# Kernel tuning notes

Measured on AMD Instinct MI355X. Metric: run time of the kernel, lower is better.

## Reference

```python
import jax, jax.numpy as jnp
import numpy as np

HEADS = 16
DIM_HEAD = 64


def setup_inputs() -> dict:
    key = jax.random.key(0)
    k1, k2, k3, k4 = jax.random.split(key, 4)
    b, sq, skv, dim = 2, 2048, 2048, 1024
    inner = HEADS * DIM_HEAD
    return {
        "x_q": jax.random.normal(k1, (b, sq, dim), dtype=jnp.float32),
        "x_kv": jax.random.normal(k2, (b, skv, dim), dtype=jnp.float32),
        "W_qkv": jax.random.normal(k3, (dim, 3 * inner), dtype=jnp.float32) * (dim ** -0.5),
        "W_out": jax.random.normal(k4, (inner, dim), dtype=jnp.float32) * (inner ** -0.5),
        "b_out": jnp.zeros((dim,), dtype=jnp.float32),
    }


def reference(x_q, x_kv, W_qkv, W_out, b_out):
    b, sq, dim = x_q.shape
    skv = x_kv.shape[1]
    inner = HEADS * DIM_HEAD
    scale = DIM_HEAD ** -0.5
    # to_qkv on concat([x_q, x_kv], seq) as in the original (bias-free linear)
    qkv = jnp.concatenate([x_q, x_kv], axis=1) @ W_qkv  # [b, sq+skv, 3*inner]
    q, k, v = jnp.split(qkv, 3, axis=-1)
    q = q[:, :sq].reshape(b, sq, HEADS, DIM_HEAD).transpose(0, 2, 1, 3)   # [b,h,sq,d]
    k = k[:, sq:].reshape(b, skv, HEADS, DIM_HEAD).transpose(0, 2, 1, 3)  # [b,h,skv,d]
    v = v[:, sq:].reshape(b, skv, HEADS, DIM_HEAD).transpose(0, 2, 1, 3)  # [b,h,skv,d]
    dots = jnp.einsum('bhqd,bhkd->bhqk', q, k) * scale
    attn = jax.nn.softmax(dots, axis=-1)  # dropout p=0.0 -> identity
    out = jnp.einsum('bhqk,bhkd->bhqd', attn, v)
    out = out.transpose(0, 2, 1, 3).reshape(b, sq, inner)
    return out @ W_out + b_out
```

## Files before the change

kernel.cpp:

```cpp
#include <hip/hip_runtime.h>


typedef __attribute__((ext_vector_type(8))) short short8;
typedef __attribute__((ext_vector_type(4))) short short4v;
typedef __attribute__((ext_vector_type(4))) float floatx4;
typedef __attribute__((ext_vector_type(16))) float floatx16;

#define QSCALE 0.18033688f

#if __has_builtin(__builtin_amdgcn_exp2f)
#define EXP2(x) __builtin_amdgcn_exp2f(x)
#else
#define EXP2(x) exp2f(x)
#endif

__device__ __forceinline__ ushort f2b(float f) {
  union { float f; unsigned u; } x; x.f = f;
  unsigned r = (x.u + 0x7fffu + ((x.u >> 16) & 1u)) >> 16;
  return (ushort)r;
}

__device__ __forceinline__ unsigned f2b2(float a, float b) {
  union { float f; unsigned u; } x, y; x.f = a; y.f = b;
  return __builtin_amdgcn_perm(y.u + 0x8000u, x.u + 0x8000u, 0x07060302u);
}

__device__ __forceinline__ unsigned cvtpk(float a, float b) {
  unsigned r;
  asm("v_cvt_pk_bf16_f32 %0, %1, %2" : "=v"(r) : "v"(a), "v"(b));
  return r;
}

#define GLL(gp, lp)                                                            \
  __builtin_amdgcn_global_load_lds(                                            \
      (const __attribute__((address_space(1))) void*)(gp),                     \
      (__attribute__((address_space(3))) void*)(lp), 16, 0, 0)

__global__ void prep(const float* __restrict__ xq, const float* __restrict__ xkv,
                     ushort* __restrict__ oq, ushort* __restrict__ okv,
                     const float* __restrict__ Wqkv, ushort* __restrict__ WqkvT,
                     const float* __restrict__ Wout, ushort* __restrict__ WoutT) {
  __shared__ float tile[32][33];
  int bid = blockIdx.x;
  const int n = 4096 * 1024;
  if (bid < 2048) {
    bool lo = bid < 1024;
    const float* in = lo ? xq : xkv;
    ushort* out = lo ? oq : okv;
    int b2 = lo ? bid : bid - 1024;
    int stride = 1024 * 256 * 4;
    for (int i = (b2 * 256 + (int)threadIdx.x) * 4; i < n; i += stride) {
      float4 v = *(const float4*)(in + i);
      uint2 o;
      o.x = cvtpk(v.x, v.y);
      o.y = cvtpk(v.z, v.w);
      *(uint2*)(out + i) = o;
    }
    return;
  }
  int tb = bid - 2048;
  int bx = tb & 127, by = tb >> 7;
  bool first = bx < 96;
  const float* in = first ? Wqkv : Wout;
  ushort* out = first ? WqkvT : WoutT;
  int N = first ? 3072 : 1024;
  int bxx = first ? bx : bx - 96;
  int k0 = by * 32, n0 = bxx * 32;
  {
    int row = threadIdx.x >> 3, c = threadIdx.x & 7;
    float4 v = *(const float4*)(in + (size_t)(k0 + row) * N + n0 + c * 4);
    tile[row][c * 4 + 0] = v.x;
    tile[row][c * 4 + 1] = v.y;
    tile[row][c * 4 + 2] = v.z;
    tile[row][c * 4 + 3] = v.w;
  }
  __syncthreads();
  {
    int tx2 = threadIdx.x & 15, ty2 = threadIdx.x >> 4;
#pragma unroll
    for (int i = 0; i < 2; i++) {
      int nr = ty2 + 16 * i;
      unsigned v = cvtpk(tile[2 * tx2][nr], tile[2 * tx2 + 1][nr]);
      *(unsigned*)(out + (size_t)(n0 + nr) * 1024 + k0 + 2 * tx2) = v;
    }
  }
}

__global__ __launch_bounds__(256, 3) void gemm_qkv(
    const ushort* __restrict__ Aq, const ushort* __restrict__ Akv,
    const ushort* __restrict__ Bt,
    ushort* __restrict__ Cq, ushort* __restrict__ Ck, ushort* __restrict__ Cv) {
  __shared__ __align__(16) ushort smem[17408];
  ushort* Asb = smem;
  ushort* Bsb = smem + 8192;
  int lid = blockIdx.y * 24 + blockIdx.x;
  int nid = (lid & 7) * 96 + (lid >> 3);
  int bx = nid % 24, by = nid / 24;
  const int n0 = bx * 128, m0 = by * 128;
  const ushort* A = (bx >= 8) ? Akv : Aq;
  const int t = threadIdx.x;
  const int w = t >> 6, lane = t & 63, dl = lane & 15, g = lane >> 4;
  const int wm = (w >> 1) * 64, wn = (w & 1) * 64;
  const int K = 1024;

  auto stage = [&](int buf, int k0) {
#pragma unroll
    for (int p = 0; p < 2; p++) {
      int j = t + p * 256;
      int row = j >> 2, slot = j & 3, c = (slot - row) & 3;
      GLL(A + (size_t)(m0 + row) * K + k0 + c * 8, &Asb[buf * 4096 + j * 8]);
    }
#pragma unroll
    for (int p = 0; p < 2; p++) {
      int j = t + p * 256;
      int row = j >> 2, slot = j & 3, c = (slot - row) & 3;
      GLL(Bt + (size_t)(n0 + row) * K + k0 + c * 8, &Bsb[buf * 4096 + j * 8]);
    }
  };

  const floatx4 fz = {0.f, 0.f, 0.f, 0.f};
  floatx4 acc[4][4];
#pragma unroll
  for (int i = 0; i < 4; i++)
#pragma unroll
    for (int j = 0; j < 4; j++) acc[i][j] = fz;

  stage(0, 0);
  for (int kt = 0; kt < 32; kt++) {
    int cur = kt & 1;
    __builtin_amdgcn_s_waitcnt(0);
    __syncthreads();
    if (kt + 1 < 32) stage(cur ^ 1, (kt + 1) * 32);
    short8 af[4], bf[4];
#pragma unroll
    for (int mt = 0; mt < 4; mt++) {
      int row = wm + mt * 16 + dl;
      af[mt] = *(const short8*)&Asb[cur * 4096 + row * 32 + ((g + row) & 3) * 8];
    }
#pragma unroll
    for (int nt = 0; nt < 4; nt++) {
      int row = wn + nt * 16 + dl;
      bf[nt] = *(const short8*)&Bsb[cur * 4096 + row * 32 + ((g + row) & 3) * 8];
    }
#pragma unroll
    for (int mt = 0; mt < 4; mt++)
#pragma unroll
      for (int nt = 0; nt < 4; nt++)
        acc[mt][nt] = __builtin_amdgcn_mfma_f32_16x16x32_bf16(af[mt], bf[nt], acc[mt][nt], 0, 0, 0);
  }

  if (bx < 16) {
#pragma unroll
    for (int mt = 0; mt < 4; mt++)
#pragma unroll
      for (int nt = 0; nt < 4; nt++) {
        int gcol = n0 + wn + nt * 16 + dl;
        int row0 = m0 + wm + mt * 16 + g * 4;
        if (gcol < 1024) {
#pragma unroll
          for (int r = 0; r < 4; r++)
            Cq[(size_t)(row0 + r) * 1024 + gcol] =
                (ushort)cvtpk(acc[mt][nt][r] * QSCALE, 0.f);
        } else {
#pragma unroll
          for (int r = 0; r < 4; r++)
            Ck[(size_t)(row0 + r) * 1024 + gcol - 1024] =
                (ushort)cvtpk(acc[mt][nt][r], 0.f);
        }
      }
  } else {
    __syncthreads();
#pragma unroll
    for (int mt = 0; mt < 4; mt++)
#pragma unroll
      for (int nt = 0; nt < 4; nt++) {
        int ncol = wn + nt * 16 + dl;
        int mrow = wm + mt * 16 + g * 4;
        uint2 pk;
        pk.x = cvtpk(acc[mt][nt][0], acc[mt][nt][1]);
        pk.y = cvtpk(acc[mt][nt][2], acc[mt][nt][3]);
        *(uint2*)&smem[ncol * 136 + mrow] = pk;
      }
    __syncthreads();
    int hd0 = n0 - 2048;
    int bb = m0 >> 11;
    int kv0 = m0 & 2047;
#pragma unroll
    for (int p = 0; p < 8; p++) {
      int j = t + p * 256;
      int row = j >> 4, c = j & 15;
      short8 v = *(const short8*)&smem[row * 136 + c * 8];
      *(short8*)(Cv + ((size_t)(bb * 1024 + hd0 + row)) * 2048 + kv0 + c * 8) = v;
    }
  }
}

__global__ __launch_bounds__(256, 3) void gemm_out(
    const ushort* __restrict__ A, const ushort* __restrict__ Bt,
    float* __restrict__ C, const float* __restrict__ bias) {
  __shared__ __align__(16) ushort As[2][128 * 64];
  __shared__ __align__(16) ushort Bs[2][64 * 64];
  int lid = blockIdx.y * 16 + blockIdx.x;
  int nid = (lid & 7) * 64 + (lid >> 3);
  int bx = nid & 15, by = nid >> 4;
  const int n0 = bx * 64, m0 = by * 128;
  const int t = threadIdx.x;
  const int w = t >> 6, lane = t & 63, dl = lane & 15, g = lane >> 4;
  const int wm = (w >> 1) * 64, wn = (w & 1) * 32;
  const int K = 1024;

  auto stage = [&](int buf, int k0) {
#pragma unroll
    for (int p = 0; p < 4; p++) {
      int j = t + p * 256;
      int row = j >> 3, slot = j & 7, c = (slot - row) & 7;
      GLL(A + (size_t)(m0 + row) * K + k0 + c * 8, &As[buf][j * 8]);
    }
#pragma unroll
    for (int p = 0; p < 2; p++) {
      int j = t + p * 256;
      int row = j >> 3, slot = j & 7, c = (slot - row) & 7;
      GLL(Bt + (size_t)(n0 + row) * K + k0 + c * 8, &Bs[buf][j * 8]);
    }
  };

  const floatx4 fz = {0.f, 0.f, 0.f, 0.f};
  floatx4 acc[4][2];
#pragma unroll
  for (int i = 0; i < 4; i++)
#pragma unroll
    for (int j = 0; j < 2; j++) acc[i][j] = fz;

  stage(0, 0);
  for (int kt = 0; kt < 16; kt++) {
    int cur = kt & 1;
    __builtin_amdgcn_s_waitcnt(0);
    __syncthreads();
    if (kt + 1 < 16) stage(cur ^ 1, (kt + 1) * 64);
#pragma unroll
    for (int ks = 0; ks < 2; ks++) {
      short8 af[4], bf[2];
#pragma unroll
      for (int mt = 0; mt < 4; mt++) {
        int row = wm + mt * 16 + dl;
        af[mt] = *(const short8*)&As[cur][row * 64 + ((ks * 4 + g + row) & 7) * 8];
      }
#pragma unroll
      for (int nt = 0; nt < 2; nt++) {
        int row = wn + nt * 16 + dl;
        bf[nt] = *(const short8*)&Bs[cur][row * 64 + ((ks * 4 + g + row) & 7) * 8];
      }
#pragma unroll
      for (int mt = 0; mt < 4; mt++)
#pragma unroll
        for (int nt = 0; nt < 2; nt++)
          acc[mt][nt] = __builtin_amdgcn_mfma_f32_16x16x32_bf16(af[mt], bf[nt], acc[mt][nt], 0, 0, 0);
    }
  }
#pragma unroll
  for (int mt = 0; mt < 4; mt++)
#pragma unroll
    for (int nt = 0; nt < 2; nt++) {
      int gcol = n0 + wn + nt * 16 + dl;
      int row0 = m0 + wm + mt * 16 + g * 4;
      float badd = bias[gcol];
#pragma unroll
      for (int r = 0; r < 4; r++)
        C[(size_t)(row0 + r) * 1024 + gcol] = acc[mt][nt][r] + badd;
    }
}

__global__ __launch_bounds__(512, 4) void attn(
    const ushort* __restrict__ Qb,
    const ushort* __restrict__ Kb,
    const ushort* __restrict__ Vt,
    ushort* __restrict__ Ob,
    int bh0) {
  __shared__ __align__(16) ushort Ks[2][2][64 * 64];
  __shared__ __align__(16) ushort Vs[2][2][64 * 64];

  const int bh = blockIdx.x + bh0, b = bh >> 4, h = bh & 15;
  const int q0 = blockIdx.y * 128;
  const int t = threadIdx.x, w = t >> 6, lane = t & 63;
  const int l31 = lane & 31, l5 = lane >> 5;
  const int qw = w & 3, kvh = w >> 2;
  const int th = t & 255;

  const ushort* Kg = Kb + (size_t)(b * 2048 + kvh * 1024) * 1024 + h * 64;
  const ushort* Vg = Vt + (size_t)(b * 1024 + h * 64) * 2048 + kvh * 1024;

  short8 bq[4];
  {
    int qa = q0 + qw * 32 + l31;
    const ushort* qrow = Qb + (size_t)(b * 2048 + qa) * 1024 + h * 64;
#pragma unroll
    for (int ks = 0; ks < 4; ks++)
      bq[ks] = *(const short8*)(qrow + ks * 16 + l5 * 8);
  }

  auto stageK = [&](int buf, int kv0) {
#pragma unroll
    for (int p = 0; p < 2; p++) {
      int j = th + p * 256;
      int row = j >> 3, slot = j & 7, c = (slot - row) & 7;
      GLL(Kg + (size_t)(kv0 + row) * 1024 + c * 8, &Ks[kvh][buf][j * 8]);
    }
  };
  auto stageV = [&](int buf, int kv0) {
#pragma unroll
    for (int p = 0; p < 2; p++) {
      int j = th + p * 256;
      int row = j >> 3, slot = j & 7, c = (slot - row) & 7;
      GLL(Vg + (size_t)row * 2048 + kv0 + c * 8, &Vs[kvh][buf][j * 8]);
    }
  };
  stageK(0, 0);
  stageV(0, 0);

  floatx16 o2[2];
#pragma unroll
  for (int m2 = 0; m2 < 2; m2++)
#pragma unroll
    for (int r = 0; r < 16; r++) o2[m2][r] = 0.f;
  floatx4 l4 = {0.f, 0.f, 0.f, 0.f};

  for (int it = 0; it < 16; it++) {
    int cur = it & 1;
    __builtin_amdgcn_s_waitcnt(0);
    __syncthreads();
    if (it + 1 < 16) { stageK(cur ^ 1, (it + 1) * 64); stageV(cur ^ 1, (it + 1) * 64); }

    short8 bp[4];
#pragma unroll
    for (int m2 = 0; m2 < 2; m2++) {
      floatx16 s;
#pragma unroll
      for (int r = 0; r < 16; r++) s[r] = 0.f;
      int row = m2 * 32 + l31;
      __builtin_amdgcn_s_setprio(1);
#pragma unroll
      for (int ks = 0; ks < 4; ks++) {
        short8 a = *(const short8*)
            &Ks[kvh][cur][row * 64 + ((ks * 2 + l5 + row) & 7) * 8];
        s = __builtin_amdgcn_mfma_f32_32x32x16_bf16(a, bq[ks], s, 0, 0, 0);
      }
      __builtin_amdgcn_s_setprio(0);
#pragma unroll
      for (int r = 0; r < 16; r++) s[r] = EXP2(s[r]);
#pragma unroll
      for (int r = 0; r < 16; r++) l4[r & 3] += s[r];
      unsigned pk[8];
#pragma unroll
      for (int p = 0; p < 8; p++)
        pk[p] = cvtpk(s[2 * p], s[2 * p + 1]);
#pragma unroll
      for (int hf = 0; hf < 2; hf++) {
        unsigned x0 = pk[hf * 4 + 0], y0 = pk[hf * 4 + 2];
        unsigned x1 = pk[hf * 4 + 1], y1 = pk[hf * 4 + 3];
        asm("v_permlane32_swap_b32 %0, %1" : "+v"(x0), "+v"(y0));
        asm("v_permlane32_swap_b32 %0, %1" : "+v"(x1), "+v"(y1));
        union { unsigned u[4]; short8 s8; } fu;
        fu.u[0] = x0; fu.u[1] = x1; fu.u[2] = y0; fu.u[3] = y1;
        bp[m2 * 2 + hf] = fu.s8;
      }
    }

    __builtin_amdgcn_s_setprio(1);
#pragma unroll
    for (int kt = 0; kt < 4; kt++)
#pragma unroll
      for (int m2 = 0; m2 < 2; m2++) {
        int row = m2 * 32 + l31;
        short8 av = *(const short8*)
            &Vs[kvh][cur][row * 64 + ((kt * 2 + l5 + row) & 7) * 8];
        o2[m2] = __builtin_amdgcn_mfma_f32_32x32x16_bf16(av, bp[kt], o2[m2], 0, 0, 0);
      }
    __builtin_amdgcn_s_setprio(0);
  }

  float lp = (l4[0] + l4[1]) + (l4[2] + l4[3]);

  __syncthreads();
  float2* Of = (float2*)&Ks[0][0][0];
  float*  Lf = (float*)&Vs[0][0][0];
  if (kvh == 1) {
#pragma unroll
    for (int m2 = 0; m2 < 2; m2++)
#pragma unroll
      for (int p = 0; p < 8; p++) {
        float2 v = {o2[m2][2 * p], o2[m2][2 * p + 1]};
        Of[(m2 * 8 + p) * 256 + qw * 64 + lane] = v;
      }
    Lf[qw * 64 + lane] = lp;
  }
  __syncthreads();
  if (kvh == 0) {
#pragma unroll
    for (int m2 = 0; m2 < 2; m2++)
#pragma unroll
      for (int p = 0; p < 8; p++) {
        float2 v = Of[(m2 * 8 + p) * 256 + qw * 64 + lane];
        o2[m2][2 * p] += v.x;
        o2[m2][2 * p + 1] += v.y;
      }
    lp += Lf[qw * 64 + lane];
  }
  float l = lp + __shfl_xor(lp, 32);
  float inv_l = 1.f / l;

  __syncthreads();
  ushort* Ot = &Ks[0][0][0];
  if (kvh == 0) {
    int q = qw * 32 + l31;
#pragma unroll
    for (int m2 = 0; m2 < 2; m2++)
#pragma unroll
      for (int pp = 0; pp < 4; pp++) {
        uint2 pk2;
        pk2.x = cvtpk(o2[m2][4 * pp + 0] * inv_l, o2[m2][4 * pp + 1] * inv_l);
        pk2.y = cvtpk(o2[m2][4 * pp + 2] * inv_l, o2[m2][4 * pp + 3] * inv_l);
        int s = m2 * 8 + 2 * pp + l5;
        *(uint2*)&Ot[q * 64 + ((s + q) & 15) * 4] = pk2;
      }
  }
  asm volatile("" ::: "memory");
  if (kvh == 0) {
#pragma unroll
    for (int p = 0; p < 4; p++) {
      int j = lane + p * 64;
      int r32 = j >> 3, c = j & 7;
      int qr = qw * 32 + r32;
      short4v lo = *(const short4v*)&Ot[qr * 64 + ((2 * c + qr) & 15) * 4];
      short4v hi = *(const short4v*)&Ot[qr * 64 + ((2 * c + 1 + qr) & 15) * 4];
      short8 v = {lo.x, lo.y, lo.z, lo.w, hi.x, hi.y, hi.z, hi.w};
      *(short8*)(Ob + (size_t)(b * 2048 + q0 + qr) * 1024 + h * 64 + c * 8) = v;
    }
  }
}

extern "C" void kernel_launch(void* const* d_in, const int* in_sizes, int n_in,
                              void* d_out, int out_size, void* d_ws, size_t ws_size,
                              hipStream_t stream) {
  const float* x_q  = (const float*)d_in[0];
  const float* x_kv = (const float*)d_in[1];
  const float* Wqkv = (const float*)d_in[2];
  const float* Wout = (const float*)d_in[3];
  const float* bout = (const float*)d_in[4];
  float* out = (float*)d_out;

  char* p = (char*)d_ws;
  ushort* Xq    = (ushort*)p; p += (size_t)4096 * 1024 * 2;
  ushort* Xkv   = (ushort*)p; p += (size_t)4096 * 1024 * 2;
  ushort* WqkvT = (ushort*)p; p += (size_t)3072 * 1024 * 2;
  ushort* WoutT = (ushort*)p; p += (size_t)1024 * 1024 * 2;
  ushort* Qb    = (ushort*)p; p += (size_t)4096 * 1024 * 2;
  ushort* Kb    = (ushort*)p; p += (size_t)4096 * 1024 * 2;
  ushort* Vt    = (ushort*)p; p += (size_t)2 * 1024 * 2048 * 2;
  ushort* Ob    = (ushort*)p; p += (size_t)4096 * 1024 * 2;

  prep<<<6144, 256, 0, stream>>>(x_q, x_kv, Xq, Xkv, Wqkv, WqkvT, Wout, WoutT);
  gemm_qkv<<<dim3(24, 32), 256, 0, stream>>>(Xq, Xkv, WqkvT, Qb, Kb, Vt);
  attn<<<dim3(16, 16), 512, 0, stream>>>(Qb, Kb, Vt, Ob, 0);
  attn<<<dim3(16, 16), 512, 0, stream>>>(Qb, Kb, Vt, Ob, 16);
  gemm_out<<<dim3(16, 32), 256, 0, stream>>>(Ob, WoutT, out, bout);
}
```

Before: 204.2 us.

## Triple-buffer GEMM loads with partial vmcnt waits and merge attention launches

```diff
diff --git a/kernel.cpp b/kernel.cpp
--- a/kernel.cpp
+++ b/kernel.cpp
@@ -18,11 +18,6 @@
   union { float f; unsigned u; } x; x.f = f;
   unsigned r = (x.u + 0x7fffu + ((x.u >> 16) & 1u)) >> 16;
   return (ushort)r;
-}
-
-__device__ __forceinline__ unsigned f2b2(float a, float b) {
-  union { float f; unsigned u; } x, y; x.f = a; y.f = b;
-  return __builtin_amdgcn_perm(y.u + 0x8000u, x.u + 0x8000u, 0x07060302u);
 }
 
 __device__ __forceinline__ unsigned cvtpk(float a, float b) {
@@ -90,9 +85,9 @@
     const ushort* __restrict__ Aq, const ushort* __restrict__ Akv,
     const ushort* __restrict__ Bt,
     ushort* __restrict__ Cq, ushort* __restrict__ Ck, ushort* __restrict__ Cv) {
-  __shared__ __align__(16) ushort smem[17408];
+  __shared__ __align__(16) ushort smem[24576];
   ushort* Asb = smem;
-  ushort* Bsb = smem + 8192;
+  ushort* Bsb = smem + 12288;
   int lid = blockIdx.y * 24 + blockIdx.x;
   int nid = (lid & 7) * 96 + (lid >> 3);
   int bx = nid % 24, by = nid / 24;
@@ -126,11 +121,17 @@
     for (int j = 0; j < 4; j++) acc[i][j] = fz;
 
   stage(0, 0);
+  stage(1, 32);
+  int cur = 0;
   for (int kt = 0; kt < 32; kt++) {
-    int cur = kt & 1;
-    __builtin_amdgcn_s_waitcnt(0);
-    __syncthreads();
-    if (kt + 1 < 32) stage(cur ^ 1, (kt + 1) * 32);
+    if (kt + 1 < 32) asm volatile("s_waitcnt vmcnt(4)" ::: "memory");
+    else             asm volatile("s_waitcnt vmcnt(0)" ::: "memory");
+    __builtin_amdgcn_s_barrier();
+    __builtin_amdgcn_sched_barrier(0);
+    if (kt + 2 < 32) {
+      int nb = (cur >= 1) ? cur - 1 : cur + 2;
+      stage(nb, (kt + 2) * 32);
+    }
     short8 af[4], bf[4];
 #pragma unroll
     for (int mt = 0; mt < 4; mt++) {
@@ -147,6 +148,7 @@
 #pragma unroll
       for (int nt = 0; nt < 4; nt++)
         acc[mt][nt] = __builtin_amdgcn_mfma_f32_16x16x32_bf16(af[mt], bf[nt], acc[mt][nt], 0, 0, 0);
+    cur = (cur < 2) ? cur + 1 : 0;
   }
 
   if (bx < 16) {
@@ -198,8 +200,9 @@
 __global__ __launch_bounds__(256, 3) void gemm_out(
     const ushort* __restrict__ A, const ushort* __restrict__ Bt,
     float* __restrict__ C, const float* __restrict__ bias) {
-  __shared__ __align__(16) ushort As[2][128 * 64];
-  __shared__ __align__(16) ushort Bs[2][64 * 64];
+  __shared__ __align__(16) ushort smem[18432];
+  ushort* As3 = smem;
+  ushort* Bs3 = smem + 12288;
   int lid = blockIdx.y * 16 + blockIdx.x;
   int nid = (lid & 7) * 64 + (lid >> 3);
   int bx = nid & 15, by = nid >> 4;
@@ -211,16 +214,15 @@
 
   auto stage = [&](int buf, int k0) {
 #pragma unroll
-    for (int p = 0; p < 4; p++) {
-      int j = t + p * 256;
-      int row = j >> 3, slot = j & 7, c = (slot - row) & 7;
-      GLL(A + (size_t)(m0 + row) * K + k0 + c * 8, &As[buf][j * 8]);
-    }
-#pragma unroll
     for (int p = 0; p < 2; p++) {
       int j = t + p * 256;
-      int row = j >> 3, slot = j & 7, c = (slot - row) & 7;
-      GLL(Bt + (size_t)(n0 + row) * K + k0 + c * 8, &Bs[buf][j * 8]);
+      int row = j >> 2, slot = j & 3, c = (slot - row) & 3;
+      GLL(A + (size_t)(m0 + row) * K + k0 + c * 8, &As3[buf * 4096 + j * 8]);
+    }
+    {
+      int j = t;
+      int row = j >> 2, slot = j & 3, c = (slot - row) & 3;
+      GLL(Bt + (size_t)(n0 + row) * K + k0 + c * 8, &Bs3[buf * 2048 + j * 8]);
     }
   };
 
@@ -232,30 +234,34 @@
     for (int j = 0; j < 2; j++) acc[i][j] = fz;
 
   stage(0, 0);
-  for (int kt = 0; kt < 16; kt++) {
-    int cur = kt & 1;
-    __builtin_amdgcn_s_waitcnt(0);
-    __syncthreads();
-    if (kt + 1 < 16) stage(cur ^ 1, (kt + 1) * 64);
-#pragma unroll
-    for (int ks = 0; ks < 2; ks++) {
-      short8 af[4], bf[2];
-#pragma unroll
-      for (int mt = 0; mt < 4; mt++) {
-        int row = wm + mt * 16 + dl;
-        af[mt] = *(const short8*)&As[cur][row * 64 + ((ks * 4 + g + row) & 7) * 8];
-      }
-#pragma unroll
-      for (int nt = 0; nt < 2; nt++) {
-        int row = wn + nt * 16 + dl;
-        bf[nt] = *(const short8*)&Bs[cur][row * 64 + ((ks * 4 + g + row) & 7) * 8];
-      }
-#pragma unroll
-      for (int mt = 0; mt < 4; mt++)
-#pragma unroll
-        for (int nt = 0; nt < 2; nt++)
-          acc[mt][nt] = __builtin_amdgcn_mfma_f32_16x16x32_bf16(af[mt], bf[nt], acc[mt][nt], 0, 0, 0);
-    }
+  stage(1, 32);
+  int cur = 0;
+  for (int kt = 0; kt < 32; kt++) {
+    if (kt + 1 < 32) asm volatile("s_waitcnt vmcnt(3)" ::: "memory");
+    else             asm volatile("s_waitcnt vmcnt(0)" ::: "memory");
+    __builtin_amdgcn_s_barrier();
+    __builtin_amdgcn_sched_barrier(0);
+    if (kt + 2 < 32) {
+      int nb = (cur >= 1) ? cur - 1 : cur + 2;
+      stage(nb, (kt + 2) * 32);
+    }
+    short8 af[4], bf[2];
+#pragma unroll
+    for (int mt = 0; mt < 4; mt++) {
+      int row = wm + mt * 16 + dl;
+      af[mt] = *(const short8*)&As3[cur * 4096 + row * 32 + ((g + row) & 3) * 8];
+    }
+#pragma unroll
+    for (int nt = 0; nt < 2; nt++) {
+      int row = wn + nt * 16 + dl;
+      bf[nt] = *(const short8*)&Bs3[cur * 2048 + row * 32 + ((g + row) & 3) * 8];
+    }
+#pragma unroll
+    for (int mt = 0; mt < 4; mt++)
+#pragma unroll
+      for (int nt = 0; nt < 2; nt++)
+        acc[mt][nt] = __builtin_amdgcn_mfma_f32_16x16x32_bf16(af[mt], bf[nt], acc[mt][nt], 0, 0, 0);
+    cur = (cur < 2) ? cur + 1 : 0;
   }
 #pragma unroll
   for (int mt = 0; mt < 4; mt++)
@@ -274,12 +280,11 @@
     const ushort* __restrict__ Qb,
     const ushort* __restrict__ Kb,
     const ushort* __restrict__ Vt,
-    ushort* __restrict__ Ob,
-    int bh0) {
+    ushort* __restrict__ Ob) {
   __shared__ __align__(16) ushort Ks[2][2][64 * 64];
   __shared__ __align__(16) ushort Vs[2][2][64 * 64];
 
-  const int bh = blockIdx.x + bh0, b = bh >> 4, h = bh & 15;
+  const int bh = blockIdx.x, b = bh >> 4, h = bh & 15;
   const int q0 = blockIdx.y * 128;
   const int t = threadIdx.x, w = t >> 6, lane = t & 63;
   const int l31 = lane & 31, l5 = lane >> 5;
@@ -460,7 +465,6 @@
 
   prep<<<6144, 256, 0, stream>>>(x_q, x_kv, Xq, Xkv, Wqkv, WqkvT, Wout, WoutT);
   gemm_qkv<<<dim3(24, 32), 256, 0, stream>>>(Xq, Xkv, WqkvT, Qb, Kb, Vt);
-  attn<<<dim3(16, 16), 512, 0, stream>>>(Qb, Kb, Vt, Ob, 0);
-  attn<<<dim3(16, 16), 512, 0, stream>>>(Qb, Kb, Vt, Ob, 16);
+  attn<<<dim3(32, 16), 512, 0, stream>>>(Qb, Kb, Vt, Ob);
   gemm_out<<<dim3(16, 32), 256, 0, stream>>>(Ob, WoutT, out, bout);
 }
```

Measured after the change: 182.9 us. 10.4% less time.
